# Kernel optimization log

Measured on AMD Instinct MI355X. Metric: run time of the kernel, lower is better.

## Reference

```python
import jax, jax.numpy as jnp
import numpy as np

B, S, HID, HEADS = 8, 1024, 1024, 16
DK = HID // HEADS


def setup_inputs() -> dict:
    key = jax.random.key(0)
    ks = jax.random.split(key, 6)
    scale = 1.0 / np.sqrt(HID)
    return {
        "q": jax.random.normal(ks[0], (B, S, HID), jnp.float32),
        "k": jax.random.normal(ks[1], (B, S, HID), jnp.float32),
        "v": jax.random.normal(ks[2], (B, S, HID), jnp.float32),
        "Wq": jax.random.normal(ks[3], (HID, HID), jnp.float32) * scale,
        "Wk": jax.random.normal(ks[4], (HID, HID), jnp.float32) * scale,
        "Wv": jax.random.normal(ks[5], (HID, HID), jnp.float32) * scale,
        "mask": 1,
    }


def _split_heads(x):
    # [B, S, HID] -> [B, HEADS, S, DK]
    b, s, _ = x.shape
    return x.reshape(b, s, HEADS, DK).transpose(0, 2, 1, 3)


def reference(q, k, v, Wq, Wk, Wv, mask):
    # torch nn.Linear: y = x @ W.T (no bias)
    qh = _split_heads(q @ Wq.T)
    kh = _split_heads(k @ Wk.T)
    vh = _split_heads(v @ Wv.T)

    scores = jnp.einsum("bhqd,bhkd->bhqk", qh, kh) / jnp.sqrt(jnp.asarray(DK, qh.dtype))
    scores = jax.nn.softmax(scores, axis=-1)
    if mask:
        # original zeroes entries where row > col AFTER softmax (keeps upper triangle)
        tri = jnp.triu(jnp.ones((S, S), scores.dtype))
        scores = scores * tri
        # original then transposes the (masked) score matrix before applying to V
        scores = scores.transpose(0, 1, 3, 2)
    out = jnp.einsum("bhqk,bhkd->bhqd", scores, vh)
    # [B, HEADS, S, DK] -> [B, S, HID]
    return out.transpose(0, 2, 1, 3).reshape(q.shape[0], -1, HID)
```

## Files before the change

### kernel.cpp

```cpp
#include <hip/hip_runtime.h>
#include <math.h>

#define B 8
#define S 1024
#define HID 1024
#define HEADS 16
#define DK 64

typedef unsigned short u16;
typedef unsigned int u32;
typedef _Float16 f16;
typedef __attribute__((ext_vector_type(8))) _Float16 half8;
typedef __attribute__((ext_vector_type(4))) _Float16 half4;
typedef __attribute__((ext_vector_type(4))) float f32x4;

#define GLL16(G, L)                                                         \
    __builtin_amdgcn_global_load_lds(                                       \
        (const __attribute__((address_space(1))) u32*)(G),                  \
        (__attribute__((address_space(3))) u32*)(L), 16, 0, 0)

__device__ __forceinline__ float exp_s(float c) {
#if __has_builtin(__builtin_amdgcn_exp2f)
    return __builtin_amdgcn_exp2f(c * 0.18033688f);
#else
    return __expf(c * 0.125f);
#endif
}

__global__ __launch_bounds__(256) void cast_fused(const float* __restrict__ x,
                                                  const float* __restrict__ w,
                                                  f16* __restrict__ xo,
                                                  f16* __restrict__ wo) {
    const size_t NX = (size_t)B * S * HID / 8;
    const size_t NW = (size_t)HID * HID / 8;
    size_t i = (size_t)blockIdx.x * 256 + threadIdx.x;
    const float* src;
    f16* dst;
    if (i < NX) { src = x + i * 8; dst = xo + i * 8; }
    else if (i < NX + NW) { src = w + (i - NX) * 8; dst = wo + (i - NX) * 8; }
    else return;
    f32x4 a = *(const f32x4*)src;
    f32x4 b = *(const f32x4*)(src + 4);
    half8 h;
    h[0] = (f16)a[0]; h[1] = (f16)a[1]; h[2] = (f16)a[2]; h[3] = (f16)a[3];
    h[4] = (f16)b[0]; h[5] = (f16)b[1]; h[6] = (f16)b[2]; h[7] = (f16)b[3];
    *(half8*)dst = h;
}

template <bool VT>
__global__ __launch_bounds__(256) void proj_mfma(const f16* __restrict__ X,
                                                 const f16* __restrict__ W,
                                                 f16* __restrict__ Y) {
    __shared__ u16 As[128 * 32];
    __shared__ u16 Bs[128 * 32];
    const int tid = threadIdx.x;
    const int wv = tid >> 6, ln = tid & 63;
    const int lr = ln & 15, quad = ln >> 4;
    const int wm = wv >> 1, wn = wv & 1;
    const int row0 = blockIdx.y * 128, col0 = blockIdx.x * 128;

    const int srow = tid >> 2;
    const int sch = tid & 3;

    f32x4 acc[4][4];
    #pragma unroll
    for (int i = 0; i < 4; ++i)
        #pragma unroll
        for (int j = 0; j < 4; ++j) acc[i][j] = (f32x4){0.f, 0.f, 0.f, 0.f};

    for (int k0 = 0; k0 < HID; k0 += 32) {
        #pragma unroll
        for (int p = 0; p < 2; ++p) {
            int r = p * 64 + srow;
            int csw = sch ^ ((r >> 1) & 3);
            GLL16(X + (size_t)(row0 + r) * HID + k0 + csw * 8, As + p * 2048 + tid * 8);
            GLL16(W + (size_t)(col0 + r) * HID + k0 + csw * 8, Bs + p * 2048 + tid * 8);
        }
        __syncthreads();
        half8 a[4], b[4];
        #pragma unroll
        for (int mi = 0; mi < 4; ++mi) {
            int r = wm * 64 + mi * 16 + lr;
            a[mi] = *(const half8*)(As + r * 32 + ((quad ^ ((r >> 1) & 3)) * 8));
        }
        #pragma unroll
        for (int ni = 0; ni < 4; ++ni) {
            int r = wn * 64 + ni * 16 + lr;
            b[ni] = *(const half8*)(Bs + r * 32 + ((quad ^ ((r >> 1) & 3)) * 8));
        }
        #pragma unroll
        for (int mi = 0; mi < 4; ++mi)
            #pragma unroll
            for (int ni = 0; ni < 4; ++ni)
                acc[mi][ni] = __builtin_amdgcn_mfma_f32_16x16x32_f16(
                    a[mi], b[ni], acc[mi][ni], 0, 0, 0);
        __syncthreads();
    }

    if (!VT) {
        #pragma unroll
        for (int mi = 0; mi < 4; ++mi) {
            int m = row0 + wm * 64 + mi * 16 + quad * 4;
            #pragma unroll
            for (int ni = 0; ni < 4; ++ni) {
                int n = col0 + wn * 64 + ni * 16 + lr;
                #pragma unroll
                for (int r = 0; r < 4; ++r)
                    Y[(size_t)(m + r) * HID + n] = (f16)acc[mi][ni][r];
            }
        }
    } else {
        #pragma unroll
        for (int mi = 0; mi < 4; ++mi) {
            int m = row0 + wm * 64 + mi * 16 + quad * 4;
            int bb = m >> 10, s = m & 1023;
            #pragma unroll
            for (int ni = 0; ni < 4; ++ni) {
                int n = col0 + wn * 64 + ni * 16 + lr;
                half4 h4;
                #pragma unroll
                for (int r = 0; r < 4; ++r) h4[r] = (f16)acc[mi][ni][r];
                *(half4*)(Y + ((size_t)(bb * 16 + (n >> 6)) * 64 + (n & 63)) * S + s) = h4;
            }
        }
    }
}

__global__ __launch_bounds__(256) void stats_mfma(const f16* __restrict__ Q,
                                                  const f16* __restrict__ K,
                                                  float* __restrict__ rlOut) {
    const int bh = blockIdx.x, jt = blockIdx.y;
    const int b = bh >> 4, h = bh & 15;
    const int tid = threadIdx.x;
    const int wv = tid >> 6, ln = tid & 63;
    const int lr = ln & 15, quad = ln >> 4;
    __shared__ u16 Qs[128 * 64];
    __shared__ u16 Ks[64 * 64];

    #pragma unroll
    for (int p = 0; p < 4; ++p) {
        int r = p * 32 + (tid >> 3);
        int csw = (tid & 7) ^ (r & 7);
        GLL16(Q + (size_t)(b * S + jt * 128 + r) * HID + h * 64 + csw * 8,
              Qs + p * 2048 + tid * 8);
    }
    __syncthreads();
    half8 aq[2][2];
    #pragma unroll
    for (int jsub = 0; jsub < 2; ++jsub) {
        int j = wv * 32 + jsub * 16 + lr;
        #pragma unroll
        for (int kf = 0; kf < 2; ++kf)
            aq[jsub][kf] = *(const half8*)(Qs + j * 64 + (((kf * 4 + quad) ^ (j & 7)) * 8));
    }

    float sl[2][4] = {};

    for (int i0 = 0; i0 < S; i0 += 64) {
        __syncthreads();
        #pragma unroll
        for (int p = 0; p < 2; ++p) {
            int r = p * 32 + (tid >> 3);
            int csw = (tid & 7) ^ (r & 7);
            GLL16(K + (size_t)(b * S + i0 + r) * HID + h * 64 + csw * 8,
                  Ks + p * 2048 + tid * 8);
        }
        __syncthreads();
        #pragma unroll
        for (int isub = 0; isub < 4; ++isub) {
            int il = isub * 16 + lr;
            half8 bk0 = *(const half8*)(Ks + il * 64 + (((0 + quad) ^ (il & 7)) * 8));
            half8 bk1 = *(const half8*)(Ks + il * 64 + (((4 + quad) ^ (il & 7)) * 8));
            #pragma unroll
            for (int jsub = 0; jsub < 2; ++jsub) {
                f32x4 c = {0.f, 0.f, 0.f, 0.f};
                c = __builtin_amdgcn_mfma_f32_16x16x32_f16(aq[jsub][0], bk0, c, 0, 0, 0);
                c = __builtin_amdgcn_mfma_f32_16x16x32_f16(aq[jsub][1], bk1, c, 0, 0, 0);
                #pragma unroll
                for (int r = 0; r < 4; ++r) sl[jsub][r] += exp_s(c[r]);
            }
        }
    }

    #pragma unroll
    for (int jsub = 0; jsub < 2; ++jsub)
        #pragma unroll
        for (int r = 0; r < 4; ++r) {
            float v = sl[jsub][r];
            v += __shfl_xor(v, 1, 64);
            v += __shfl_xor(v, 2, 64);
            v += __shfl_xor(v, 4, 64);
            v += __shfl_xor(v, 8, 64);
            if (lr == 0)
                rlOut[(size_t)bh * S + jt * 128 + wv * 32 + jsub * 16 + quad * 4 + r] =
                    1.0f / v;
        }
}

__global__ __launch_bounds__(256) void apply_mfma(const f16* __restrict__ Q,
                                                  const f16* __restrict__ K,
                                                  const f16* __restrict__ Vt,
                                                  const float* __restrict__ rlS,
                                                  float* __restrict__ out) {
    const int bh = blockIdx.x;
    const int it2 = (gridDim.y - 1) - blockIdx.y;
    const int b = bh >> 4, h = bh & 15;
    const int tid = threadIdx.x;
    const int wv = tid >> 6, ln = tid & 63;
    const int lr = ln & 15, quad = ln >> 4;
    const int i0b = it2 * 128;

    __shared__ u16 Qs[32 * 64];
    __shared__ u16 Vts[64 * 32];

    half8 bk[2][2];
    #pragma unroll
    for (int isub = 0; isub < 2; ++isub) {
        int i = i0b + wv * 32 + isub * 16 + lr;
        #pragma unroll
        for (int kf = 0; kf < 2; ++kf)
            bk[isub][kf] = *(const half8*)(K + (size_t)(b * S + i) * HID + h * 64 +
                                           kf * 32 + quad * 8);
    }

    f32x4 acc[4][2];
    #pragma unroll
    for (int nt = 0; nt < 4; ++nt)
        #pragma unroll
        for (int isub = 0; isub < 2; ++isub) acc[nt][isub] = (f32x4){0.f, 0.f, 0.f, 0.f};

    const int nch = 4 * it2 + 4;
    for (int jc = 0; jc < nch; ++jc) {
        const int j0 = jc * 32;
        __syncthreads();
        {
            int r = tid >> 3, csw = (tid & 7) ^ (r & 7);
            GLL16(Q + (size_t)(b * S + j0 + r) * HID + h * 64 + csw * 8, Qs + tid * 8);
        }
        {
            int d = tid >> 2, cph = (tid & 3) ^ ((d >> 1) & 3);
            GLL16(Vt + (size_t)(bh * 64 + d) * S + j0 + cph * 8, Vts + tid * 8);
        }
        __syncthreads();

        #pragma unroll
        for (int jsub = 0; jsub < 2; ++jsub) {
            const int jbase = j0 + jsub * 16;
            const int ib0 = i0b + wv * 32;
            if (jbase > ib0 + 16 + 15) continue;

            const int jl = jsub * 16 + lr;
            half8 aq0 = *(const half8*)(Qs + jl * 64 + (((0 + quad) ^ (jl & 7)) * 8));
            half8 aq1 = *(const half8*)(Qs + jl * 64 + (((4 + quad) ^ (jl & 7)) * 8));
            half4 av[4];
            #pragma unroll
            for (int nt = 0; nt < 4; ++nt) {
                int d = nt * 16 + lr;
                int ph = (jsub * 2 + (quad >> 1)) ^ ((d >> 1) & 3);
                av[nt] = *(const half4*)(Vts + d * 32 + ph * 8 + (quad & 1) * 4);
            }
            f32x4 rl4 = *(const f32x4*)(rlS + (size_t)bh * S + jbase + quad * 4);

            #pragma unroll
            for (int isub = 0; isub < 2; ++isub) {
                const int ib = ib0 + isub * 16;
                if (jbase > ib + 15) continue;
                f32x4 c = {0.f, 0.f, 0.f, 0.f};
                c = __builtin_amdgcn_mfma_f32_16x16x32_f16(aq0, bk[isub][0], c, 0, 0, 0);
                c = __builtin_amdgcn_mfma_f32_16x16x32_f16(aq1, bk[isub][1], c, 0, 0, 0);
                const bool nm = (jbase + 15 > ib);
                const int i_col = ib + lr;
                half4 bw;
                #pragma unroll
                for (int r = 0; r < 4; ++r) {
                    float w = exp_s(c[r]) * rl4[r];
                    if (nm) {
                        int j = jbase + quad * 4 + r;
                        if (j > i_col) w = 0.f;
                    }
                    bw[r] = (f16)w;
                }
                #pragma unroll
                for (int nt = 0; nt < 4; ++nt)
                    acc[nt][isub] = __builtin_amdgcn_mfma_f32_16x16x16f16(
                        av[nt], bw, acc[nt][isub], 0, 0, 0);
            }
        }
    }

    #pragma unroll
    for (int isub = 0; isub < 2; ++isub) {
        int i = i0b + wv * 32 + isub * 16 + lr;
        #pragma unroll
        for (int nt = 0; nt < 4; ++nt)
            *(f32x4*)(out + (size_t)(b * S + i) * HID + h * 64 + nt * 16 + quad * 4) =
                acc[nt][isub];
    }
}

extern "C" void kernel_launch(void* const* d_in, const int* in_sizes, int n_in,
                              void* d_out, int out_size, void* d_ws, size_t ws_size,
                              hipStream_t stream) {
    const float* q  = (const float*)d_in[0];
    const float* k  = (const float*)d_in[1];
    const float* v  = (const float*)d_in[2];
    const float* Wq = (const float*)d_in[3];
    const float* Wk = (const float*)d_in[4];
    const float* Wv = (const float*)d_in[5];

    const size_t SZ = (size_t)B * S * HID;
    const size_t WZ = (size_t)HID * HID;

    char* p = (char*)d_ws;
    f16* xb = (f16*)p;      p += SZ * 2;
    f16* wb = (f16*)p;      p += WZ * 2;
    f16* Qb = (f16*)p;      p += SZ * 2;
    f16* Kb = (f16*)p;      p += SZ * 2;
    f16* Vt = (f16*)p;      p += SZ * 2;
    float* rlS = (float*)p;

    float* out = (float*)d_out;

    const int ncast = (int)((SZ + WZ) / 8 + 255) / 256;
    dim3 gproj(HID / 128, (B * S) / 128);

    cast_fused<<<ncast, 256, 0, stream>>>(q, Wq, xb, wb);
    proj_mfma<false><<<gproj, 256, 0, stream>>>(xb, wb, Qb);

    cast_fused<<<ncast, 256, 0, stream>>>(k, Wk, xb, wb);
    proj_mfma<false><<<gproj, 256, 0, stream>>>(xb, wb, Kb);

    cast_fused<<<ncast, 256, 0, stream>>>(v, Wv, xb, wb);
    proj_mfma<true><<<gproj, 256, 0, stream>>>(xb, wb, Vt);

    stats_mfma<<<dim3(B * HEADS, S / 128), 256, 0, stream>>>(Qb, Kb, rlS);
    apply_mfma<<<dim3(B * HEADS, S / 128), 256, 0, stream>>>(Qb, Kb, Vt, rlS, out);
}
```

Measured before the change: 318.2 us.

## Fold softmax row normalizer into V and enlarge attention tiles

The stats kernel now handles 256 query rows per block and, instead of writing reciprocal row sums to a buffer, scales the transposed V columns in place by those reciprocals. The apply kernel therefore drops its per-chunk normalizer load and multiply. It also processes 64-wide j chunks with larger shared tiles, which halves the barrier count, and packs weights to fp16 with cvt_pkrtz. The trade-offs are that the stats kernel launches half as many blocks, it does an extra read-modify-write pass over V, and folding the scale into fp16 V before the matmul changes rounding.

After: 317.6 us. About the same (-0.2%).

```diff
diff --git a/kernel.cpp b/kernel.cpp
--- a/kernel.cpp
+++ b/kernel.cpp
@@ -12,6 +12,8 @@
 typedef _Float16 f16;
 typedef __attribute__((ext_vector_type(8))) _Float16 half8;
 typedef __attribute__((ext_vector_type(4))) _Float16 half4;
+typedef __attribute__((ext_vector_type(2))) _Float16 half2;
+typedef __attribute__((ext_vector_type(2))) __fp16 fp16x2;
 typedef __attribute__((ext_vector_type(4))) float f32x4;
 
 #define GLL16(G, L)                                                         \
@@ -128,33 +130,34 @@
 
 __global__ __launch_bounds__(256) void stats_mfma(const f16* __restrict__ Q,
                                                   const f16* __restrict__ K,
-                                                  float* __restrict__ rlOut) {
+                                                  f16* __restrict__ Vt) {
     const int bh = blockIdx.x, jt = blockIdx.y;
     const int b = bh >> 4, h = bh & 15;
     const int tid = threadIdx.x;
     const int wv = tid >> 6, ln = tid & 63;
     const int lr = ln & 15, quad = ln >> 4;
-    __shared__ u16 Qs[128 * 64];
+    __shared__ u16 Qs[256 * 64];
     __shared__ u16 Ks[64 * 64];
-
-    #pragma unroll
-    for (int p = 0; p < 4; ++p) {
+    __shared__ float rlL[256];
+
+    #pragma unroll
+    for (int p = 0; p < 8; ++p) {
         int r = p * 32 + (tid >> 3);
         int csw = (tid & 7) ^ (r & 7);
-        GLL16(Q + (size_t)(b * S + jt * 128 + r) * HID + h * 64 + csw * 8,
+        GLL16(Q + (size_t)(b * S + jt * 256 + r) * HID + h * 64 + csw * 8,
               Qs + p * 2048 + tid * 8);
     }
     __syncthreads();
-    half8 aq[2][2];
-    #pragma unroll
-    for (int jsub = 0; jsub < 2; ++jsub) {
-        int j = wv * 32 + jsub * 16 + lr;
+    half8 aq[4][2];
+    #pragma unroll
+    for (int jsub = 0; jsub < 4; ++jsub) {
+        int j = wv * 64 + jsub * 16 + lr;
         #pragma unroll
         for (int kf = 0; kf < 2; ++kf)
             aq[jsub][kf] = *(const half8*)(Qs + j * 64 + (((kf * 4 + quad) ^ (j & 7)) * 8));
     }
 
-    float sl[2][4] = {};
+    float sl[4][4] = {};
 
     for (int i0 = 0; i0 < S; i0 += 64) {
         __syncthreads();
@@ -172,7 +175,7 @@
             half8 bk0 = *(const half8*)(Ks + il * 64 + (((0 + quad) ^ (il & 7)) * 8));
             half8 bk1 = *(const half8*)(Ks + il * 64 + (((4 + quad) ^ (il & 7)) * 8));
             #pragma unroll
-            for (int jsub = 0; jsub < 2; ++jsub) {
+            for (int jsub = 0; jsub < 4; ++jsub) {
                 f32x4 c = {0.f, 0.f, 0.f, 0.f};
                 c = __builtin_amdgcn_mfma_f32_16x16x32_f16(aq[jsub][0], bk0, c, 0, 0, 0);
                 c = __builtin_amdgcn_mfma_f32_16x16x32_f16(aq[jsub][1], bk1, c, 0, 0, 0);
@@ -183,7 +186,7 @@
     }
 
     #pragma unroll
-    for (int jsub = 0; jsub < 2; ++jsub)
+    for (int jsub = 0; jsub < 4; ++jsub)
         #pragma unroll
         for (int r = 0; r < 4; ++r) {
             float v = sl[jsub][r];
@@ -192,15 +195,27 @@
             v += __shfl_xor(v, 4, 64);
             v += __shfl_xor(v, 8, 64);
             if (lr == 0)
-                rlOut[(size_t)bh * S + jt * 128 + wv * 32 + jsub * 16 + quad * 4 + r] =
-                    1.0f / v;
-        }
+                rlL[wv * 64 + jsub * 16 + quad * 4 + r] = 1.0f / v;
+        }
+    __syncthreads();
+
+    {
+        const int d = tid >> 2, cg = (tid & 3) * 64;
+        f16* vrow = Vt + (size_t)(bh * 64 + d) * S + jt * 256 + cg;
+        #pragma unroll
+        for (int c8 = 0; c8 < 8; ++c8) {
+            half8 hv = *(half8*)(vrow + c8 * 8);
+            #pragma unroll
+            for (int e = 0; e < 8; ++e)
+                hv[e] = (f16)((float)hv[e] * rlL[cg + c8 * 8 + e]);
+            *(half8*)(vrow + c8 * 8) = hv;
+        }
+    }
 }
 
 __global__ __launch_bounds__(256) void apply_mfma(const f16* __restrict__ Q,
                                                   const f16* __restrict__ K,
                                                   const f16* __restrict__ Vt,
-                                                  const float* __restrict__ rlS,
                                                   float* __restrict__ out) {
     const int bh = blockIdx.x;
     const int it2 = (gridDim.y - 1) - blockIdx.y;
@@ -209,14 +224,15 @@
     const int wv = tid >> 6, ln = tid & 63;
     const int lr = ln & 15, quad = ln >> 4;
     const int i0b = it2 * 128;
-
-    __shared__ u16 Qs[32 * 64];
-    __shared__ u16 Vts[64 * 32];
+    const int i0w = i0b + wv * 32;
+
+    __shared__ u16 Qs[64 * 64];
+    __shared__ u16 Vts[64 * 64];
 
     half8 bk[2][2];
     #pragma unroll
     for (int isub = 0; isub < 2; ++isub) {
-        int i = i0b + wv * 32 + isub * 16 + lr;
+        int i = i0w + isub * 16 + lr;
         #pragma unroll
         for (int kf = 0; kf < 2; ++kf)
             bk[isub][kf] = *(const half8*)(K + (size_t)(b * S + i) * HID + h * 64 +
@@ -229,25 +245,30 @@
         #pragma unroll
         for (int isub = 0; isub < 2; ++isub) acc[nt][isub] = (f32x4){0.f, 0.f, 0.f, 0.f};
 
-    const int nch = 4 * it2 + 4;
+    const int nch = 2 * it2 + 2;
     for (int jc = 0; jc < nch; ++jc) {
-        const int j0 = jc * 32;
-        __syncthreads();
-        {
-            int r = tid >> 3, csw = (tid & 7) ^ (r & 7);
-            GLL16(Q + (size_t)(b * S + j0 + r) * HID + h * 64 + csw * 8, Qs + tid * 8);
-        }
-        {
-            int d = tid >> 2, cph = (tid & 3) ^ ((d >> 1) & 3);
-            GLL16(Vt + (size_t)(bh * 64 + d) * S + j0 + cph * 8, Vts + tid * 8);
-        }
-        __syncthreads();
-
-        #pragma unroll
-        for (int jsub = 0; jsub < 2; ++jsub) {
+        const int j0 = jc * 64;
+        __syncthreads();
+        #pragma unroll
+        for (int p = 0; p < 2; ++p) {
+            int r = p * 32 + (tid >> 3);
+            int csw = (tid & 7) ^ (r & 7);
+            GLL16(Q + (size_t)(b * S + j0 + r) * HID + h * 64 + csw * 8,
+                  Qs + p * 2048 + tid * 8);
+        }
+        #pragma unroll
+        for (int p = 0; p < 2; ++p) {
+            int d = p * 32 + (tid >> 3);
+            int csw = (tid & 7) ^ (d & 7);
+            GLL16(Vt + (size_t)(bh * 64 + d) * S + j0 + csw * 8,
+                  Vts + p * 2048 + tid * 8);
+        }
+        __syncthreads();
+
+        #pragma unroll
+        for (int jsub = 0; jsub < 4; ++jsub) {
             const int jbase = j0 + jsub * 16;
-            const int ib0 = i0b + wv * 32;
-            if (jbase > ib0 + 16 + 15) continue;
+            if (jbase > i0w + 31) break;
 
             const int jl = jsub * 16 + lr;
             half8 aq0 = *(const half8*)(Qs + jl * 64 + (((0 + quad) ^ (jl & 7)) * 8));
@@ -256,30 +277,33 @@
             #pragma unroll
             for (int nt = 0; nt < 4; ++nt) {
                 int d = nt * 16 + lr;
-                int ph = (jsub * 2 + (quad >> 1)) ^ ((d >> 1) & 3);
-                av[nt] = *(const half4*)(Vts + d * 32 + ph * 8 + (quad & 1) * 4);
-            }
-            f32x4 rl4 = *(const f32x4*)(rlS + (size_t)bh * S + jbase + quad * 4);
+                int ch = (jsub * 2 + (quad >> 1)) ^ (d & 7);
+                av[nt] = *(const half4*)(Vts + d * 64 + ch * 8 + (quad & 1) * 4);
+            }
 
             #pragma unroll
             for (int isub = 0; isub < 2; ++isub) {
-                const int ib = ib0 + isub * 16;
+                const int ib = i0w + isub * 16;
                 if (jbase > ib + 15) continue;
                 f32x4 c = {0.f, 0.f, 0.f, 0.f};
                 c = __builtin_amdgcn_mfma_f32_16x16x32_f16(aq0, bk[isub][0], c, 0, 0, 0);
                 c = __builtin_amdgcn_mfma_f32_16x16x32_f16(aq1, bk[isub][1], c, 0, 0, 0);
-                const bool nm = (jbase + 15 > ib);
-                const int i_col = ib + lr;
+                float w0 = exp_s(c[0]), w1 = exp_s(c[1]);
+                float w2 = exp_s(c[2]), w3 = exp_s(c[3]);
+                if (jbase + 15 > ib) {
+                    const int i_col = ib + lr;
+                    const int jq = jbase + quad * 4;
+                    if (jq + 0 > i_col) w0 = 0.f;
+                    if (jq + 1 > i_col) w1 = 0.f;
+                    if (jq + 2 > i_col) w2 = 0.f;
+                    if (jq + 3 > i_col) w3 = 0.f;
+                }
+                fp16x2 q0 = __builtin_amdgcn_cvt_pkrtz(w0, w1);
+                fp16x2 q1 = __builtin_amdgcn_cvt_pkrtz(w2, w3);
+                half2 p0 = __builtin_bit_cast(half2, q0);
+                half2 p1 = __builtin_bit_cast(half2, q1);
                 half4 bw;
-                #pragma unroll
-                for (int r = 0; r < 4; ++r) {
-                    float w = exp_s(c[r]) * rl4[r];
-                    if (nm) {
-                        int j = jbase + quad * 4 + r;
-                        if (j > i_col) w = 0.f;
-                    }
-                    bw[r] = (f16)w;
-                }
+                bw[0] = p0[0]; bw[1] = p0[1]; bw[2] = p1[0]; bw[3] = p1[1];
                 #pragma unroll
                 for (int nt = 0; nt < 4; ++nt)
                     acc[nt][isub] = __builtin_amdgcn_mfma_f32_16x16x16f16(
@@ -290,7 +314,7 @@
 
     #pragma unroll
     for (int isub = 0; isub < 2; ++isub) {
-        int i = i0b + wv * 32 + isub * 16 + lr;
+        int i = i0w + isub * 16 + lr;
         #pragma unroll
         for (int nt = 0; nt < 4; ++nt)
             *(f32x4*)(out + (size_t)(b * S + i) * HID + h * 64 + nt * 16 + quad * 4) =
@@ -317,7 +341,6 @@
     f16* Qb = (f16*)p;      p += SZ * 2;
     f16* Kb = (f16*)p;      p += SZ * 2;
     f16* Vt = (f16*)p;      p += SZ * 2;
-    float* rlS = (float*)p;
 
     float* out = (float*)d_out;
 
@@ -333,6 +356,6 @@
     cast_fused<<<ncast, 256, 0, stream>>>(v, Wv, xb, wb);
     proj_mfma<true><<<gproj, 256, 0, stream>>>(xb, wb, Vt);
 
-    stats_mfma<<<dim3(B * HEADS, S / 128), 256, 0, stream>>>(Qb, Kb, rlS);
-    apply_mfma<<<dim3(B * HEADS, S / 128), 256, 0, stream>>>(Qb, Kb, Vt, rlS, out);
-}
+    stats_mfma<<<dim3(B * HEADS, S / 256), 256, 0, stream>>>(Qb, Kb, Vt);
+    apply_mfma<<<dim3(B * HEADS, S / 128), 256, 0, stream>>>(Qb, Kb, Vt, out);
+}
```
